# Performance work log

Measured on AMD Instinct MI355X. Metric: run time of the kernel, lower is better.

Reference implementation:

```python
import jax, jax.numpy as jnp
import numpy as np

B, T, E, WIN, OC, VOCAB = 256, 2048, 128, 5, 128, 50000


def setup_inputs() -> dict:
    key = jax.random.key(0)
    k1, k2, k3, k4, k5, k6 = jax.random.split(key, 6)
    return {
        "x": jax.random.randint(k1, (B, T), 0, VOCAB + 1, dtype=jnp.int32),
        "emb_table": jax.random.normal(k2, (VOCAB + 1, E), dtype=jnp.float32),
        "att_w": jax.random.normal(k3, (WIN, E), dtype=jnp.float32) * 0.05,
        "att_b": jax.random.normal(k4, (1,), dtype=jnp.float32),
        "cnn_w": jax.random.normal(k5, (OC, E), dtype=jnp.float32) * 0.05,
        "cnn_b": jax.random.normal(k6, (OC,), dtype=jnp.float32),
    }


def reference(x, emb_table, att_w, att_b, cnn_w, cnn_b):
    win = att_w.shape[0]
    pad = (win - 1) // 2
    embed = emb_table[x]                                   # [B, T, E]
    x_pad = jnp.pad(embed, ((0, 0), (pad, pad), (0, 0)))
    T_ = embed.shape[1]
    # Sliding-window dot product over full embed dim (the degenerate Conv2d)
    s = jnp.zeros(embed.shape[:2], dtype=embed.dtype)      # [B, T]
    for k in range(win):
        s = s + jnp.einsum('bte,e->bt', x_pad[:, k:k + T_, :], att_w[k])
    scores = jax.nn.sigmoid(s + att_b[0])                  # [B, T]
    gated = embed * scores[:, :, None]                     # [B, T, E]
    feat = jnp.tanh(jnp.einsum('bte,oe->bto', gated, cnn_w) + cnn_b)  # [B, T, OC]
    out = jnp.max(feat, axis=1)                            # [B, OC] (maxpool over seq)
    return out[:, :, None, None]                           # [B, OC, 1, 1]
```

## Files before the change

kernel.cpp:

```cpp
#include <hip/hip_runtime.h>
#include <hip/hip_bf16.h>
#include <math.h>

#define B_   256
#define T_   2048
#define E_   128
#define WIN_ 5
#define PAD_ 2
#define OC_  128
#define VOCAB_MAX 50000
#define VOCAB1 50001
#define TT   64
#define REAL_ROWS (TT + WIN_ - 1)
#define ROWS 80
#define ASTR 136
#define VROWS 64
#define BT   512

typedef __attribute__((ext_vector_type(8))) short short8;
typedef __attribute__((ext_vector_type(4))) float floatx4;
typedef __attribute__((ext_vector_type(4))) unsigned uintx4;

static __device__ __forceinline__ short f2bf(float f) {
    union { __hip_bfloat16 h; short s; } u;
    u.h = __float2bfloat16(f);
    return u.s;
}

__device__ __forceinline__ void atomicMaxFloat(float* addr, float v) {
    if (v >= 0.0f) atomicMax((int*)addr, __float_as_int(v));
    else           atomicMin((unsigned int*)addr, __float_as_uint(v));
}

__launch_bounds__(256, 4)
__global__ void build_tables(const float* __restrict__ emb,
                             const float* __restrict__ cnn_w,
                             const float* __restrict__ att_w,
                             short* __restrict__ D,
                             float* __restrict__ r,
                             float* __restrict__ out) {
    __shared__ short sh_a[VROWS * ASTR];

    const int tid  = threadIdx.x;
    const int lane = tid & 63;
    const int w    = tid >> 6;
    const int l15  = lane & 15;
    const int quad = lane >> 4;
    const int v0   = blockIdx.x * VROWS;

    if (blockIdx.x < (B_ * OC_) / 256)
        out[blockIdx.x * 256 + tid] = -INFINITY;

    #pragma unroll
    for (int t = 0; t < 8; t++) {
        int i   = t * 256 + tid;
        int row = i >> 5, c4 = i & 31;
        int vr  = v0 + row; if (vr > VOCAB_MAX) vr = VOCAB_MAX;
        float4 v = *(const float4*)(emb + (size_t)vr * E_ + c4 * 4);
        short4 o; o.x = f2bf(v.x); o.y = f2bf(v.y); o.z = f2bf(v.z); o.w = f2bf(v.w);
        *(short4*)(&sh_a[row * ASTR + c4 * 4]) = o;
    }

    short8 Bf[2][4];
    #pragma unroll
    for (int j = 0; j < 2; j++)
        #pragma unroll
        for (int ks = 0; ks < 4; ks++) {
            const float4* p = (const float4*)(cnn_w + (size_t)(w * 32 + j * 16 + l15) * E_ + ks * 32 + quad * 8);
            float4 p0 = p[0], p1 = p[1];
            Bf[j][ks] = (short8){ f2bf(p0.x), f2bf(p0.y), f2bf(p0.z), f2bf(p0.w),
                                  f2bf(p1.x), f2bf(p1.y), f2bf(p1.z), f2bf(p1.w) };
        }

    short8 Ba[4];
    #pragma unroll
    for (int ks = 0; ks < 4; ks++) {
        short8 v = (short8){0,0,0,0,0,0,0,0};
        if (l15 < WIN_) {
            const float4* p = (const float4*)(att_w + (size_t)l15 * E_ + ks * 32 + quad * 8);
            float4 p0 = p[0], p1 = p[1];
            v = (short8){ f2bf(p0.x), f2bf(p0.y), f2bf(p0.z), f2bf(p0.w),
                          f2bf(p1.x), f2bf(p1.y), f2bf(p1.z), f2bf(p1.w) };
        }
        Ba[ks] = v;
    }
    __syncthreads();

    #pragma unroll
    for (int mt = 0; mt < 4; mt++) {
        short8 a[4];
        #pragma unroll
        for (int ks = 0; ks < 4; ks++)
            a[ks] = *(const short8*)(&sh_a[(mt * 16 + l15) * ASTR + ks * 32 + quad * 8]);
        #pragma unroll
        for (int j = 0; j < 2; j++) {
            floatx4 acc = (floatx4){0.f, 0.f, 0.f, 0.f};
            #pragma unroll
            for (int ks = 0; ks < 4; ks++)
                acc = __builtin_amdgcn_mfma_f32_16x16x32_bf16(a[ks], Bf[j][ks], acc, 0, 0, 0);
            #pragma unroll
            for (int rr = 0; rr < 4; rr++) {
                int v = v0 + mt * 16 + quad * 4 + rr;
                if (v <= VOCAB_MAX)
                    D[(size_t)v * E_ + w * 32 + j * 16 + l15] = f2bf(acc[rr]);
            }
        }
    }

    {
        short8 a[4];
        #pragma unroll
        for (int ks = 0; ks < 4; ks++)
            a[ks] = *(const short8*)(&sh_a[(w * 16 + l15) * ASTR + ks * 32 + quad * 8]);
        floatx4 acc = (floatx4){0.f, 0.f, 0.f, 0.f};
        #pragma unroll
        for (int ks = 0; ks < 4; ks++)
            acc = __builtin_amdgcn_mfma_f32_16x16x32_bf16(a[ks], Ba[ks], acc, 0, 0, 0);
        if (l15 < 8) {
            #pragma unroll
            for (int rr = 0; rr < 4; rr++) {
                int v = v0 + w * 16 + quad * 4 + rr;
                if (v <= VOCAB_MAX) r[(size_t)v * 8 + l15] = acc[rr];
            }
        }
    }
}

__launch_bounds__(256, 6)
__global__ void score_max(const int* __restrict__ x,
                          const short* __restrict__ D,
                          const float* __restrict__ r,
                          const float* __restrict__ att_b_p,
                          const float* __restrict__ cnn_b,
                          float* __restrict__ out) {
    __shared__ int   sh_x[BT + 4];
    __shared__ float sh_rt[WIN_][BT + 8];
    __shared__ float sh_sc[BT];
    __shared__ float sh_red[4][128];

    const int tid  = threadIdx.x;
    const int lane = tid & 63;
    const int w    = tid >> 6;
    const int b    = blockIdx.y;
    const int t0   = blockIdx.x * BT;
    const int l15  = lane & 15;
    const int grp  = lane >> 4;

    for (int i = tid; i < BT + 4; i += 256) {
        int t = t0 + i - PAD_;
        sh_x[i] = (t >= 0 && t < T_) ? x[b * T_ + t] : -1;
    }
    __syncthreads();

    for (int i = tid; i < BT + 4; i += 256) {
        int v = sh_x[i];
        float4 r03 = make_float4(0.f, 0.f, 0.f, 0.f);
        float  r4  = 0.f;
        if (v >= 0) {
            r03 = *(const float4*)(r + (size_t)v * 8);
            r4  = r[(size_t)v * 8 + 4];
        }
        sh_rt[0][i] = r03.x; sh_rt[1][i] = r03.y; sh_rt[2][i] = r03.z;
        sh_rt[3][i] = r03.w; sh_rt[4][i] = r4;
    }
    __syncthreads();

    {
        const float attb = att_b_p[0];
        #pragma unroll
        for (int rep = 0; rep < 2; rep++) {
            int j = rep * 256 + tid;
            float s = attb;
            #pragma unroll
            for (int k = 0; k < WIN_; k++) s += sh_rt[k][j + k];
            sh_sc[j] = 1.0f / (1.0f + __expf(-s));
        }
    }
    __syncthreads();

    float mm[8];
    #pragma unroll
    for (int c = 0; c < 8; c++) mm[c] = -INFINITY;

    const int base_t = w * 128;
    for (int batch = 0; batch < 4; batch++) {
        uintx4 u[8];
        float  sc8[8];
        const int start = base_t + batch * 32;
        #pragma unroll
        for (int j = 0; j < 8; j++) {
            int tok = start + j * 4 + grp;
            int v   = sh_x[tok + PAD_];
            sc8[j]  = sh_sc[tok];
            u[j]    = *(const uintx4*)(D + (size_t)v * E_ + l15 * 8);
        }
        #pragma unroll
        for (int j = 0; j < 8; j++) {
            #pragma unroll
            for (int q = 0; q < 4; q++) {
                float lo = __uint_as_float(u[j][q] << 16);
                float hi = __uint_as_float(u[j][q] & 0xFFFF0000u);
                mm[q * 2]     = fmaxf(mm[q * 2],     sc8[j] * lo);
                mm[q * 2 + 1] = fmaxf(mm[q * 2 + 1], sc8[j] * hi);
            }
        }
    }
    #pragma unroll
    for (int c = 0; c < 8; c++) {
        mm[c] = fmaxf(mm[c], __shfl_xor(mm[c], 16));
        mm[c] = fmaxf(mm[c], __shfl_xor(mm[c], 32));
    }
    if (lane < 16) {
        #pragma unroll
        for (int c = 0; c < 8; c++) sh_red[w][l15 * 8 + c] = mm[c];
    }
    __syncthreads();
    if (tid < 128) {
        float m = fmaxf(fmaxf(sh_red[0][tid], sh_red[1][tid]),
                        fmaxf(sh_red[2][tid], sh_red[3][tid]));
        atomicMaxFloat(&out[b * OC_ + tid], tanhf(m + cnn_b[tid]));
    }
}

__global__ void prep_small(const float* __restrict__ cnn_w, const float* __restrict__ att_w,
                           short* __restrict__ wsw, short* __restrict__ wsatt) {
    int i = blockIdx.x * 256 + threadIdx.x;
    if (i < OC_ * E_)  wsw[i]   = f2bf(cnn_w[i]);
    if (i < WIN_ * E_) wsatt[i] = f2bf(att_w[i]);
}

__launch_bounds__(256, 4)
__global__ void fallback_main(const int* __restrict__ x,
                              const float* __restrict__ emb,
                              const float* __restrict__ att_b_p,
                              const short* __restrict__ wsw,
                              const short* __restrict__ wsatt,
                              const float* __restrict__ cnn_b,
                              float* __restrict__ out) {
    __shared__ short sh_a[ROWS * ASTR];
    __shared__ short sh_att[16 * ASTR];
    __shared__ float sh_r[ROWS * 8];
    __shared__ float sh_score[TT];
    __shared__ int   sh_idx[8 * ROWS];

    const int tid  = threadIdx.x;
    const int lane = tid & 63;
    const int w    = tid >> 6;
    const int b    = blockIdx.y;
    const int t0   = blockIdx.x * (8 * TT);
    const int l15  = lane & 15;
    const int quad = lane >> 4;
    const int rbase = tid >> 4;
    const int c     = tid & 15;

    for (int i = tid; i < 8 * ROWS; i += 256) {
        int tile = i / ROWS, row = i - tile * ROWS;
        int t = t0 + tile * TT + row - PAD_;
        sh_idx[i] = (row < REAL_ROWS && t >= 0 && t < T_) ? x[b * T_ + t] : -1;
    }
    {
        int o = tid >> 4, cc = tid & 15;
        short8 v = (short8){0,0,0,0,0,0,0,0};
        if (o < WIN_) v = *(const short8*)(wsatt + o * E_ + cc * 8);
        *(short8*)(&sh_att[o * ASTR + cc * 8]) = v;
    }
    short8 Bf[2][4];
    #pragma unroll
    for (int j = 0; j < 2; j++)
        #pragma unroll
        for (int ks = 0; ks < 4; ks++)
            Bf[j][ks] = *(const short8*)(wsw + (size_t)(w * 32 + j * 16 + l15) * E_ + ks * 32 + quad * 8);
    __syncthreads();

    short8 g[5];
    #pragma unroll
    for (int k = 0; k < 5; k++) {
        int idx = sh_idx[rbase + 16 * k];
        short8 v = (short8){0,0,0,0,0,0,0,0};
        if (idx >= 0) {
            const float4* p = (const float4*)(emb + (size_t)idx * E_ + c * 8);
            float4 p0 = p[0], p1 = p[1];
            v = (short8){ f2bf(p0.x), f2bf(p0.y), f2bf(p0.z), f2bf(p0.w),
                          f2bf(p1.x), f2bf(p1.y), f2bf(p1.z), f2bf(p1.w) };
        }
        g[k] = v;
    }
    #pragma unroll
    for (int k = 0; k < 5; k++)
        *(short8*)(&sh_a[(rbase + 16 * k) * ASTR + c * 8]) = g[k];
    __syncthreads();

    const float attb = att_b_p[0];
    float mm[2] = { -INFINITY, -INFINITY };

    for (int it = 0; it < 8; it++) {
        for (int mt = w; mt < 5; mt += 4) {
            floatx4 acc = (floatx4){0.f, 0.f, 0.f, 0.f};
            #pragma unroll
            for (int ks = 0; ks < 4; ks++) {
                short8 a  = *(const short8*)(&sh_a[(mt * 16 + l15) * ASTR + ks * 32 + quad * 8]);
                short8 bs = *(const short8*)(&sh_att[l15 * ASTR + ks * 32 + quad * 8]);
                acc = __builtin_amdgcn_mfma_f32_16x16x32_bf16(a, bs, acc, 0, 0, 0);
            }
            if (l15 < 8) {
                #pragma unroll
                for (int r = 0; r < 4; r++)
                    sh_r[(mt * 16 + quad * 4 + r) * 8 + l15] = acc[r];
            }
        }
        __syncthreads();

        if (it + 1 < 8) {
            const int* idxp = &sh_idx[(it + 1) * ROWS];
            #pragma unroll
            for (int k = 0; k < 5; k++) {
                int idx = idxp[rbase + 16 * k];
                short8 v = (short8){0,0,0,0,0,0,0,0};
                if (idx >= 0) {
                    const float4* p = (const float4*)(emb + (size_t)idx * E_ + c * 8);
                    float4 p0 = p[0], p1 = p[1];
                    v = (short8){ f2bf(p0.x), f2bf(p0.y), f2bf(p0.z), f2bf(p0.w),
                                  f2bf(p1.x), f2bf(p1.y), f2bf(p1.z), f2bf(p1.w) };
                }
                g[k] = v;
            }
        }

        if (tid < TT) {
            float s = attb;
            #pragma unroll
            for (int k = 0; k < WIN_; k++) s += sh_r[(tid + k) * 8 + k];
            sh_score[tid] = 1.0f / (1.0f + __expf(-s));
        }

        floatx4 acc[4][2];
        #pragma unroll
        for (int i = 0; i < 4; i++)
            #pragma unroll
            for (int j = 0; j < 2; j++) acc[i][j] = (floatx4){0.f, 0.f, 0.f, 0.f};
        #pragma unroll
        for (int ks = 0; ks < 4; ks++) {
            int ko = ks * 32 + quad * 8;
            #pragma unroll
            for (int i = 0; i < 4; i++) {
                short8 ai = *(const short8*)(&sh_a[(PAD_ + i * 16 + l15) * ASTR + ko]);
                acc[i][0] = __builtin_amdgcn_mfma_f32_16x16x32_bf16(ai, Bf[0][ks], acc[i][0], 0, 0, 0);
                acc[i][1] = __builtin_amdgcn_mfma_f32_16x16x32_bf16(ai, Bf[1][ks], acc[i][1], 0, 0, 0);
            }
        }
        __syncthreads();

        #pragma unroll
        for (int i = 0; i < 4; i++) {
            #pragma unroll
            for (int r = 0; r < 4; r++) {
                float sc = sh_score[i * 16 + quad * 4 + r];
                mm[0] = fmaxf(mm[0], sc * acc[i][0][r]);
                mm[1] = fmaxf(mm[1], sc * acc[i][1][r]);
            }
        }

        if (it + 1 < 8) {
            #pragma unroll
            for (int k = 0; k < 5; k++)
                *(short8*)(&sh_a[(rbase + 16 * k) * ASTR + c * 8]) = g[k];
            __syncthreads();
        }
    }

    #pragma unroll
    for (int j = 0; j < 2; j++) {
        float m = mm[j];
        m = fmaxf(m, __shfl_xor(m, 16));
        m = fmaxf(m, __shfl_xor(m, 32));
        if (lane < 16) {
            int o = w * 32 + j * 16 + lane;
            atomicMaxFloat(&out[b * OC_ + o], tanhf(m + cnn_b[o]));
        }
    }
}

extern "C" void kernel_launch(void* const* d_in, const int* in_sizes, int n_in,
                              void* d_out, int out_size, void* d_ws, size_t ws_size,
                              hipStream_t stream) {
    const int*   x     = (const int*)d_in[0];
    const float* emb   = (const float*)d_in[1];
    const float* att_w = (const float*)d_in[2];
    const float* att_b = (const float*)d_in[3];
    const float* cnn_w = (const float*)d_in[4];
    const float* cnn_b = (const float*)d_in[5];
    float* out = (float*)d_out;

    const size_t d_elems = (size_t)VOCAB1 * E_;
    const size_t r_elems = (size_t)VOCAB1 * 8;
    const size_t need = d_elems * 2 + r_elems * 4 + 64;

    if (ws_size >= need) {
        short* Dt = (short*)d_ws;
        float* rt = (float*)(Dt + d_elems);
        build_tables<<<(VOCAB1 + VROWS - 1) / VROWS, 256, 0, stream>>>(emb, cnn_w, att_w, Dt, rt, out);
        dim3 grid(T_ / BT, B_);
        score_max<<<grid, 256, 0, stream>>>(x, Dt, rt, att_b, cnn_b, out);
    } else {
        hipMemsetAsync(d_out, 0xFF, (size_t)B_ * OC_ * sizeof(float), stream);
        short* ws_w   = (short*)d_ws;
        short* ws_att = ws_w + OC_ * E_;
        prep_small<<<16, 256, 0, stream>>>(cnn_w, att_w, ws_w, ws_att);
        dim3 grid(T_ / (8 * TT), B_);
        fallback_main<<<grid, 256, 0, stream>>>(x, emb, att_b, ws_w, ws_att, cnn_b, out);
    }
}
```

Measured before the change: 109.9 us.

## Stage D table stores through LDS and double-buffer gather loads in score_max

build_tables now writes its MFMA results into a shared-memory tile and then stores D with coalesced 16-byte row writes, replacing scattered 2-byte global stores. score_max merges the token and r-table load loops, dropping one barrier. It also software-pipelines the D-row gathers so the next batch's loads are issued before the current batch is reduced. The first gather is also moved ahead of the sigmoid score computation. The extra register buffers lead to lowering score_max's launch bound from 6 to 4 waves, trading occupancy for more memory-level parallelism.

```diff
diff --git a/kernel.cpp b/kernel.cpp
--- a/kernel.cpp
+++ b/kernel.cpp
@@ -40,6 +40,7 @@
                              float* __restrict__ r,
                              float* __restrict__ out) {
     __shared__ short sh_a[VROWS * ASTR];
+    __shared__ short sh_d[VROWS * ASTR];
 
     const int tid  = threadIdx.x;
     const int lane = tid & 63;
@@ -99,11 +100,8 @@
             for (int ks = 0; ks < 4; ks++)
                 acc = __builtin_amdgcn_mfma_f32_16x16x32_bf16(a[ks], Bf[j][ks], acc, 0, 0, 0);
             #pragma unroll
-            for (int rr = 0; rr < 4; rr++) {
-                int v = v0 + mt * 16 + quad * 4 + rr;
-                if (v <= VOCAB_MAX)
-                    D[(size_t)v * E_ + w * 32 + j * 16 + l15] = f2bf(acc[rr]);
-            }
+            for (int rr = 0; rr < 4; rr++)
+                sh_d[(mt * 16 + quad * 4 + rr) * ASTR + w * 32 + j * 16 + l15] = f2bf(acc[rr]);
         }
     }
 
@@ -124,9 +122,20 @@
             }
         }
     }
-}
-
-__launch_bounds__(256, 6)
+    __syncthreads();
+
+    #pragma unroll
+    for (int st = 0; st < 4; st++) {
+        int i   = st * 256 + tid;
+        int row = i >> 4, c = i & 15;
+        int v   = v0 + row;
+        if (v <= VOCAB_MAX)
+            *(short8*)(D + (size_t)v * E_ + c * 8) =
+                *(const short8*)(&sh_d[row * ASTR + c * 8]);
+    }
+}
+
+__launch_bounds__(256, 4)
 __global__ void score_max(const int* __restrict__ x,
                           const short* __restrict__ D,
                           const float* __restrict__ r,
@@ -148,12 +157,8 @@
 
     for (int i = tid; i < BT + 4; i += 256) {
         int t = t0 + i - PAD_;
-        sh_x[i] = (t >= 0 && t < T_) ? x[b * T_ + t] : -1;
-    }
-    __syncthreads();
-
-    for (int i = tid; i < BT + 4; i += 256) {
-        int v = sh_x[i];
+        int v = (t >= 0 && t < T_) ? x[b * T_ + t] : -1;
+        sh_x[i] = v;
         float4 r03 = make_float4(0.f, 0.f, 0.f, 0.f);
         float  r4  = 0.f;
         if (v >= 0) {
@@ -165,6 +170,16 @@
     }
     __syncthreads();
 
+    const int base_t = w * 128;
+
+    uintx4 uA[8];
+    #pragma unroll
+    for (int j = 0; j < 8; j++) {
+        int tok = base_t + j * 4 + grp;
+        int v   = sh_x[tok + PAD_];
+        uA[j]   = *(const uintx4*)(D + (size_t)v * E_ + l15 * 8);
+    }
+
     {
         const float attb = att_b_p[0];
         #pragma unroll
@@ -182,29 +197,39 @@
     #pragma unroll
     for (int c = 0; c < 8; c++) mm[c] = -INFINITY;
 
-    const int base_t = w * 128;
+    #pragma unroll
     for (int batch = 0; batch < 4; batch++) {
-        uintx4 u[8];
-        float  sc8[8];
+        uintx4 uB[8];
+        if (batch < 3) {
+            const int nstart = base_t + (batch + 1) * 32;
+            #pragma unroll
+            for (int j = 0; j < 8; j++) {
+                int tok = nstart + j * 4 + grp;
+                int v   = sh_x[tok + PAD_];
+                uB[j]   = *(const uintx4*)(D + (size_t)v * E_ + l15 * 8);
+            }
+        }
+
         const int start = base_t + batch * 32;
+        float sc8[8];
+        #pragma unroll
+        for (int j = 0; j < 8; j++) sc8[j] = sh_sc[start + j * 4 + grp];
+
         #pragma unroll
         for (int j = 0; j < 8; j++) {
-            int tok = start + j * 4 + grp;
-            int v   = sh_x[tok + PAD_];
-            sc8[j]  = sh_sc[tok];
-            u[j]    = *(const uintx4*)(D + (size_t)v * E_ + l15 * 8);
-        }
-        #pragma unroll
-        for (int j = 0; j < 8; j++) {
             #pragma unroll
             for (int q = 0; q < 4; q++) {
-                float lo = __uint_as_float(u[j][q] << 16);
-                float hi = __uint_as_float(u[j][q] & 0xFFFF0000u);
+                float lo = __uint_as_float(uA[j][q] << 16);
+                float hi = __uint_as_float(uA[j][q] & 0xFFFF0000u);
                 mm[q * 2]     = fmaxf(mm[q * 2],     sc8[j] * lo);
                 mm[q * 2 + 1] = fmaxf(mm[q * 2 + 1], sc8[j] * hi);
             }
         }
-    }
+
+        #pragma unroll
+        for (int j = 0; j < 8; j++) uA[j] = uB[j];
+    }
+
     #pragma unroll
     for (int c = 0; c < 8; c++) {
         mm[c] = fmaxf(mm[c], __shfl_xor(mm[c], 16));
```

New measurement: 110.5 us. No clear change (+0.5%).
